# Kernel optimization log

Measured on AMD Instinct MI355X. Metric: run time of the kernel, lower is better.

## Reference

```python
import jax, jax.numpy as jnp
import numpy as np


def setup_inputs() -> dict:
    key = jax.random.key(0)
    k1, k2, k3 = jax.random.split(key, 3)
    B, d, N, T = 8, 256, 4096, 1024
    K = jax.random.normal(k1, (B, d, N), dtype=jnp.float32)
    V = jax.random.normal(k2, (B, d, N), dtype=jnp.float32)
    Q = jax.random.normal(k3, (B, d, T), dtype=jnp.float32)
    return {"K": K, "V": V, "Q": Q}


def reference(K, V, Q):
    d = K.shape[1]
    scale = 1.0 / jnp.sqrt(jnp.asarray(d, dtype=K.dtype))
    # scores: (B, N, T) = K^T @ Q
    scores = jnp.einsum('bdn,bdt->bnt', K, Q) * scale
    A = jax.nn.softmax(scores, axis=1)  # softmax over keys N
    R = jnp.einsum('bdn,bnt->bdt', V, A)  # (B, d, T)
    R_ = jnp.concatenate((R, Q), axis=1)  # (B, 2d, T)
    maxAtt = jnp.argmax(A, axis=1)  # (B, T)
    return (R_, A, maxAtt)
```

## Files before the change

### kernel.cpp

```cpp
#include <hip/hip_runtime.h>
#include <cfloat>

#define BB 8
#define DD 256
#define NN 4096
#define TT 1024
constexpr float SCALE = 0.0625f;

typedef __attribute__((ext_vector_type(8))) short bf16x8;
typedef __attribute__((ext_vector_type(4))) float f32x4;
typedef __attribute__((ext_vector_type(8))) unsigned short u16x8;

__device__ inline unsigned short f2bf(float x) {
  union { float f; unsigned u; } v; v.f = x;
  unsigned r = v.u + 0x7fff + ((v.u >> 16) & 1);
  return (unsigned short)(r >> 16);
}
__device__ inline float bf2f(unsigned short h) {
  union { unsigned u; float f; } v; v.u = ((unsigned)h) << 16;
  return v.f;
}

__device__ inline void glds16(const unsigned short* g, const short* lbase) {
  __builtin_amdgcn_global_load_lds((const __attribute__((address_space(1))) unsigned int*)g,
                                   (__attribute__((address_space(3))) unsigned int*)lbase,
                                   16, 0, 0);
}

__device__ inline void wg_barrier() {
  __builtin_amdgcn_sched_barrier(0);
  __builtin_amdgcn_s_barrier();
  __builtin_amdgcn_sched_barrier(0);
}

#define MPART_OFF 0u
#define LPART_OFF (1u << 20)
#define IPART_OFF (2u << 20)
#define MARR_OFF  (3u << 20)
#define RLARR_OFF ((3u << 20) + 32768u)
#define CONV_OFF  (4u << 20)
#define KT_HI_OFF (CONV_OFF)
#define KT_LO_OFF (CONV_OFF + 16777216u)
#define QT_HI_OFF (CONV_OFF + 33554432u)
#define QT_LO_OFF (CONV_OFF + 37748736u)
#define VH_OFF    (CONV_OFF + 41943040u)
#define RPART_OFF (CONV_OFF)
#define WS_NEED   (62914560ull)

__global__ __launch_bounds__(256) void convert_all(const float* __restrict__ Ksrc,
                                                   const float* __restrict__ Qsrc,
                                                   const float* __restrict__ Vsrc,
                                                   unsigned short* __restrict__ KHi,
                                                   unsigned short* __restrict__ KLo,
                                                   unsigned short* __restrict__ QHi,
                                                   unsigned short* __restrict__ QLo,
                                                   unsigned short* __restrict__ Vh) {
  __shared__ float tile[64][65];
  const int bx = blockIdx.x;
  const int b = blockIdx.z;
  const int tid = threadIdx.x;

  if (bx >= 80) {
    const int y = blockIdx.y;
    size_t g = (((size_t)b * 4 + y) * 256 + (bx - 80)) * 256 + tid;
    float4 v = ((const float4*)Vsrc)[g];
    unsigned short h[4] = {f2bf(v.x), f2bf(v.y), f2bf(v.z), f2bf(v.w)};
    *(ushort4*)(Vh + g * 4) = *(ushort4*)h;
    return;
  }

  const int d0 = blockIdx.y * 64;
  const float* src; unsigned short* dhi; unsigned short* dlo; int C; int c0;
  if (bx < 64) { src = Ksrc; dhi = KHi; dlo = KLo; C = NN; c0 = bx * 64; }
  else         { src = Qsrc; dhi = QHi; dlo = QLo; C = TT; c0 = (bx - 64) * 64; }
  const float* s = src + ((size_t)b * DD + d0) * C + c0;
  const int r = tid >> 4, cg = (tid & 15) * 4;
#pragma unroll
  for (int it = 0; it < 4; ++it) {
    float4 v = *(const float4*)(s + (size_t)(r + it * 16) * C + cg);
    tile[r + it * 16][cg + 0] = v.x; tile[r + it * 16][cg + 1] = v.y;
    tile[r + it * 16][cg + 2] = v.z; tile[r + it * 16][cg + 3] = v.w;
  }
  __syncthreads();
  const int cl = tid >> 2, dg = (tid & 3) * 16;
  unsigned short hi[16], lo[16];
#pragma unroll
  for (int j = 0; j < 16; ++j) {
    float x = tile[dg + j][cl];
    unsigned short h = f2bf(x);
    hi[j] = h;
    lo[j] = f2bf(x - bf2f(h));
  }
  size_t off = ((size_t)b * C + c0 + cl) * DD + d0 + dg;
  *(u16x8*)(dhi + off) = *(u16x8*)&hi[0];
  *(u16x8*)(dhi + off + 8) = *(u16x8*)&hi[8];
  *(u16x8*)(dlo + off) = *(u16x8*)&lo[0];
  *(u16x8*)(dlo + off + 8) = *(u16x8*)&lo[8];
}

__global__ __launch_bounds__(256) void gemm_scores_mfma(const unsigned short* __restrict__ KtHi,
                                                        const unsigned short* __restrict__ KtLo,
                                                        const unsigned short* __restrict__ QtHi,
                                                        const unsigned short* __restrict__ QtLo,
                                                        float* __restrict__ S,
                                                        float* __restrict__ mPart,
                                                        float* __restrict__ lPart,
                                                        int* __restrict__ iPart) {
  __shared__ __align__(16) short sAhi[2][128 * 32];
  __shared__ __align__(16) short sAlo[2][128 * 32];
  __shared__ __align__(16) short sBhi[2][128 * 32];
  __shared__ __align__(16) short sBlo[2][128 * 32];
  __shared__ float sm[256], sl[256];
  __shared__ int si[256];

  const int lin = blockIdx.x + ((blockIdx.y + (blockIdx.z << 5)) << 3);
  const int wg = ((lin & 7) << 8) + (lin >> 3);
  const int b = wg >> 8;
  const int cy = (wg >> 3) & 31;
  const int n0 = cy * 128;
  const int t0 = (wg & 7) * 128;
  const int tid = threadIdx.x;
  const int lane = tid & 63, w = tid >> 6;
  const int nh = (w & 1) * 64, th = (w >> 1) * 64;
  const int fr = lane & 15, q = lane >> 4;

  const unsigned short* aHi = KtHi + ((size_t)b * NN + n0) * DD;
  const unsigned short* aLo = KtLo + ((size_t)b * NN + n0) * DD;
  const unsigned short* bHi = QtHi + ((size_t)b * TT + t0) * DD;
  const unsigned short* bLo = QtLo + ((size_t)b * TT + t0) * DD;

  f32x4 acc[4][4];
#pragma unroll
  for (int i = 0; i < 4; ++i)
#pragma unroll
    for (int j = 0; j < 4; ++j) acc[i][j] = (f32x4){0.f, 0.f, 0.f, 0.f};

  const int Rr = lane >> 2;
  const int Qq = (lane & 3) ^ ((lane >> 3) & 3);
  const size_t s0 = (size_t)((w * 2 + 0) * 16 + Rr) * DD + Qq * 8;
  const size_t s1 = (size_t)((w * 2 + 1) * 16 + Rr) * DD + Qq * 8;
  const int g0 = (w * 2 + 0) * 512;
  const int g1 = (w * 2 + 1) * 512;
  const int pq8 = (q ^ ((fr >> 1) & 3)) * 8;

#define STAGE_K1(buf, kk)                         \
    glds16(aHi + s0 + (kk), &sAhi[buf][g0]);      \
    glds16(aHi + s1 + (kk), &sAhi[buf][g1]);      \
    glds16(aLo + s0 + (kk), &sAlo[buf][g0]);      \
    glds16(aLo + s1 + (kk), &sAlo[buf][g1]);      \
    glds16(bHi + s0 + (kk), &sBhi[buf][g0]);      \
    glds16(bHi + s1 + (kk), &sBhi[buf][g1]);      \
    glds16(bLo + s0 + (kk), &sBlo[buf][g0]);      \
    glds16(bLo + s1 + (kk), &sBlo[buf][g1]);

  STAGE_K1(0, 0);

  for (int step = 0; step < 8; ++step) {
    const int bi = step & 1;
    if (step < 7) {
      STAGE_K1(bi ^ 1, (step + 1) * 32);
      __builtin_amdgcn_sched_barrier(0);
      asm volatile("s_waitcnt vmcnt(8)" ::: "memory");
    } else {
      __builtin_amdgcn_sched_barrier(0);
      asm volatile("s_waitcnt vmcnt(0)" ::: "memory");
    }
    wg_barrier();

    bf16x8 bh[4], bl[4];
#pragma unroll
    for (int tb = 0; tb < 4; ++tb) {
      int off = (((w >> 1) * 4 + tb) * 512) + fr * 32 + pq8;
      bh[tb] = *(const bf16x8*)&sBhi[bi][off];
      bl[tb] = *(const bf16x8*)&sBlo[bi][off];
    }
#pragma unroll
    for (int mb = 0; mb < 4; ++mb) {
      int off = (((w & 1) * 4 + mb) * 512) + fr * 32 + pq8;
      bf16x8 ah = *(const bf16x8*)&sAhi[bi][off];
      bf16x8 al = *(const bf16x8*)&sAlo[bi][off];
#pragma unroll
      for (int tb = 0; tb < 4; ++tb) {
        acc[mb][tb] = __builtin_amdgcn_mfma_f32_16x16x32_bf16(ah, bh[tb], acc[mb][tb], 0, 0, 0);
        acc[mb][tb] = __builtin_amdgcn_mfma_f32_16x16x32_bf16(ah, bl[tb], acc[mb][tb], 0, 0, 0);
        acc[mb][tb] = __builtin_amdgcn_mfma_f32_16x16x32_bf16(al, bh[tb], acc[mb][tb], 0, 0, 0);
      }
    }
    wg_barrier();
  }
#undef STAGE_K1

#pragma unroll
  for (int tb = 0; tb < 4; ++tb) {
    const int tl = th + tb * 16 + fr;
    const int t = t0 + tl;
    float tmp[16];
    float m = -FLT_MAX; int id = 0;
#pragma unroll
    for (int mb = 0; mb < 4; ++mb)
#pragma unroll
      for (int r = 0; r < 4; ++r) {
        float v = acc[mb][tb][r] * SCALE;
        int n = n0 + nh + mb * 16 + q * 4 + r;
        S[((size_t)b * NN + n) * TT + t] = v;
        tmp[mb * 4 + r] = v;
        int nl = nh + mb * 16 + q * 4 + r;
        if (v > m) { m = v; id = nl; }
      }
    float l = 0.f;
#pragma unroll
    for (int j = 0; j < 16; ++j) l += __expf(tmp[j] - m);
#pragma unroll
    for (int off = 16; off <= 32; off <<= 1) {
      float m2 = __shfl_xor(m, off);
      float l2 = __shfl_xor(l, off);
      int i2 = __shfl_xor(id, off);
      if (m2 > m)       { l = l * __expf(m - m2) + l2; m = m2; id = i2; }
      else if (m2 == m) { l += l2; id = min(id, i2); }
      else              { l += l2 * __expf(m2 - m); }
    }
    if (q == 0) {
      int slot = (w & 1) * 128 + tl;
      sm[slot] = m; sl[slot] = l; si[slot] = id;
    }
  }
  __syncthreads();
  if (tid < 128) {
    float m = sm[tid], l = sl[tid]; int id = si[tid];
    float m2 = sm[128 + tid], l2 = sl[128 + tid]; int i2 = si[128 + tid];
    if (m2 > m)       { l = l * __expf(m - m2) + l2; m = m2; id = i2; }
    else if (m2 == m) { l += l2; id = min(id, i2); }
    else              { l += l2 * __expf(m2 - m); }
    size_t p = ((size_t)b * 32 + cy) * TT + t0 + tid;
    mPart[p] = m; lPart[p] = l; iPart[p] = n0 + id;
  }
}

__global__ __launch_bounds__(256) void gemm_out_fused2(const unsigned short* __restrict__ Vh,
                                                       float* __restrict__ A,
                                                       const float* __restrict__ mPart,
                                                       const float* __restrict__ lPart,
                                                       const int* __restrict__ iPart,
                                                       float* __restrict__ Rpart,
                                                       float* __restrict__ outMax) {
  __shared__ __align__(16) short sV[2][256 * 32];
  __shared__ __align__(16) short sA[32 * 40];
  __shared__ float rsm[8][32], rsl[8][32];
  __shared__ int   rsi[8][32];
  __shared__ float sm[32], srl[32];

  const int lin = blockIdx.x + (blockIdx.y << 5) + (blockIdx.z << 7);
  const int b  = lin & 7;
  const int ny = (lin >> 3) & 3;
  const int t0 = ((lin >> 5) & 31) * 32;

  const int tid = threadIdx.x;
  const int lane = tid & 63, w = tid >> 6;
  const int fr = lane & 15, q = lane >> 4, fk = q * 8;
  const int sn = tid >> 3, tg = tid & 7;

  const unsigned short* Vb = Vh + (size_t)b * DD * NN;
  float* Ab = A + (size_t)b * NN * TT;
  float* Arow = Ab + (size_t)sn * TT + t0 + tg * 4;

  const int Rr = lane >> 2;
  const int Qq = (lane & 3) ^ ((lane >> 3) & 3);
  const unsigned short* vsrc = Vb + (size_t)(w * 64 + Rr) * NN + Qq * 8;
  const int pq8 = (q ^ ((fr >> 1) & 3)) * 8;
  const int n0 = ny * 1024;

#pragma unroll
  for (int c = 0; c < 4; ++c)
    glds16(vsrc + (size_t)(c * 16) * NN + n0, &sV[0][(w * 4 + c) * 512]);
  float4 cur = *(const float4*)(Arow + (size_t)n0 * TT);

  {
    const int tl = tid & 31, g = tid >> 5;
    float m = -FLT_MAX, l = 0.f; int idx = 0;
#pragma unroll
    for (int cc = 0; cc < 4; ++cc) {
      size_t p = ((size_t)b * 32 + g * 4 + cc) * TT + t0 + tl;
      float m2 = mPart[p], l2 = lPart[p]; int i2 = iPart[p];
      if (m2 > m)       { l = l * __expf(m - m2) + l2; m = m2; idx = i2; }
      else if (m2 == m) { l += l2; idx = min(idx, i2); }
      else              { l += l2 * __expf(m2 - m); }
    }
    rsm[g][tl] = m; rsl[g][tl] = l; rsi[g][tl] = idx;
  }
  __syncthreads();
  if (tid < 32) {
    float m = rsm[0][tid], l = rsl[0][tid]; int idx = rsi[0][tid];
#pragma unroll
    for (int g = 1; g < 8; ++g) {
      float m2 = rsm[g][tid], l2 = rsl[g][tid]; int i2 = rsi[g][tid];
      if (m2 > m)       { l = l * __expf(m - m2) + l2; m = m2; idx = i2; }
      else if (m2 == m) { l += l2; idx = min(idx, i2); }
      else              { l += l2 * __expf(m2 - m); }
    }
    sm[tid] = m; srl[tid] = 1.0f / l;
    if (ny == 0) outMax[(size_t)b * TT + t0 + tid] = (float)idx;
  }
  asm volatile("s_waitcnt vmcnt(0)" ::: "memory");
  __syncthreads();

  const float4 mv = *(const float4*)&sm[tg * 4];
  const float4 rv = *(const float4*)&srl[tg * 4];

  f32x4 acc[4][2];
#pragma unroll
  for (int i = 0; i < 4; ++i) { acc[i][0] = (f32x4){0,0,0,0}; acc[i][1] = (f32x4){0,0,0,0}; }

  for (int it = 0; it < 31; ++it) {
    const int nn = n0 + it * 32;
    const int bi = it & 1;
#pragma unroll
    for (int c = 0; c < 4; ++c)
      glds16(vsrc + (size_t)(c * 16) * NN + (nn + 32), &sV[bi ^ 1][(w * 4 + c) * 512]);
    float4 nxt = *(const float4*)(Arow + (size_t)(nn + 32) * TT);

    float4 av;
    av.x = __expf(cur.x - mv.x) * rv.x;
    av.y = __expf(cur.y - mv.y) * rv.y;
    av.z = __expf(cur.z - mv.z) * rv.z;
    av.w = __expf(cur.w - mv.w) * rv.w;
    *(float4*)(Arow + (size_t)nn * TT) = av;
    sA[(tg * 4 + 0) * 40 + sn] = (short)f2bf(av.x);
    sA[(tg * 4 + 1) * 40 + sn] = (short)f2bf(av.y);
    sA[(tg * 4 + 2) * 40 + sn] = (short)f2bf(av.z);
    sA[(tg * 4 + 3) * 40 + sn] = (short)f2bf(av.w);

    __builtin_amdgcn_sched_barrier(0);
    asm volatile("s_waitcnt vmcnt(8) lgkmcnt(0)" ::: "memory");
    wg_barrier();

    bf16x8 bf0 = *(const bf16x8*)&sA[(0 * 16 + fr) * 40 + fk];
    bf16x8 bf1 = *(const bf16x8*)&sA[(1 * 16 + fr) * 40 + fk];
#pragma unroll
    for (int mb = 0; mb < 4; ++mb) {
      bf16x8 af = *(const bf16x8*)&sV[bi][w * 2048 + mb * 512 + fr * 32 + pq8];
      acc[mb][0] = __builtin_amdgcn_mfma_f32_16x16x32_bf16(af, bf0, acc[mb][0], 0, 0, 0);
      acc[mb][1] = __builtin_amdgcn_mfma_f32_16x16x32_bf16(af, bf1, acc[mb][1], 0, 0, 0);
    }
    wg_barrier();
    cur = nxt;
  }

  {
    const int nn = n0 + 992;
    float4 av;
    av.x = __expf(cur.x - mv.x) * rv.x;
    av.y = __expf(cur.y - mv.y) * rv.y;
    av.z = __expf(cur.z - mv.z) * rv.z;
    av.w = __expf(cur.w - mv.w) * rv.w;
    *(float4*)(Arow + (size_t)nn * TT) = av;
    sA[(tg * 4 + 0) * 40 + sn] = (short)f2bf(av.x);
    sA[(tg * 4 + 1) * 40 + sn] = (short)f2bf(av.y);
    sA[(tg * 4 + 2) * 40 + sn] = (short)f2bf(av.z);
    sA[(tg * 4 + 3) * 40 + sn] = (short)f2bf(av.w);

    __builtin_amdgcn_sched_barrier(0);
    asm volatile("s_waitcnt vmcnt(0) lgkmcnt(0)" ::: "memory");
    wg_barrier();

    bf16x8 bf0 = *(const bf16x8*)&sA[(0 * 16 + fr) * 40 + fk];
    bf16x8 bf1 = *(const bf16x8*)&sA[(1 * 16 + fr) * 40 + fk];
#pragma unroll
    for (int mb = 0; mb < 4; ++mb) {
      bf16x8 af = *(const bf16x8*)&sV[1][w * 2048 + mb * 512 + fr * 32 + pq8];
      acc[mb][0] = __builtin_amdgcn_mfma_f32_16x16x32_bf16(af, bf0, acc[mb][0], 0, 0, 0);
      acc[mb][1] = __builtin_amdgcn_mfma_f32_16x16x32_bf16(af, bf1, acc[mb][1], 0, 0, 0);
    }
  }

#pragma unroll
  for (int mb = 0; mb < 4; ++mb)
#pragma unroll
    for (int tb = 0; tb < 2; ++tb) {
      const int t = t0 + tb * 16 + fr;
#pragma unroll
      for (int r = 0; r < 4; ++r) {
        const int d = w * 64 + mb * 16 + q * 4 + r;
        Rpart[(((size_t)b * 4 + ny) * DD + d) * TT + t] = acc[mb][tb][r];
      }
    }
}

__global__ __launch_bounds__(256) void combine(const float* __restrict__ Rpart,
                                               const float* __restrict__ Qp,
                                               float* __restrict__ out) {
  const int lin = blockIdx.x;
  const int b = lin & 7;
  const int d = lin >> 3;
  const int t = threadIdx.x * 4;
  if (d < 256) {
    float4 s0 = *(const float4*)(Rpart + (((size_t)b * 4 + 0) * DD + d) * TT + t);
    float4 s1 = *(const float4*)(Rpart + (((size_t)b * 4 + 1) * DD + d) * TT + t);
    float4 s2 = *(const float4*)(Rpart + (((size_t)b * 4 + 2) * DD + d) * TT + t);
    float4 s3 = *(const float4*)(Rpart + (((size_t)b * 4 + 3) * DD + d) * TT + t);
    float4 r = make_float4(s0.x + s1.x + s2.x + s3.x, s0.y + s1.y + s2.y + s3.y,
                           s0.z + s1.z + s2.z + s3.z, s0.w + s1.w + s2.w + s3.w);
    *(float4*)(out + ((size_t)b * 512 + d) * TT + t) = r;
  } else {
    float4 v = *(const float4*)(Qp + ((size_t)b * 256 + (d - 256)) * TT + t);
    *(float4*)(out + ((size_t)b * 512 + d) * TT + t) = v;
  }
}

__global__ __launch_bounds__(256) void gemm_scores_fp32(const float* __restrict__ Kp,
                                                        const float* __restrict__ Qp,
                                                        float* __restrict__ S) {
  const int b = blockIdx.z;
  const int n0 = blockIdx.y * 128;
  const int t0 = blockIdx.x * 128;
  const int tid = threadIdx.x;
  const int tx = tid & 15, ty = tid >> 4;
  __shared__ float Kt[8][128];
  __shared__ float Qt[8][128];
  float acc[8][8];
#pragma unroll
  for (int i = 0; i < 8; ++i)
#pragma unroll
    for (int j = 0; j < 8; ++j) acc[i][j] = 0.f;
  const int lin = tid * 4;
  const int lkk = lin >> 7, lcol = lin & 127;
  const float* Kbase = Kp + (size_t)b * DD * NN;
  const float* Qbase = Qp + (size_t)b * DD * TT;
  for (int dd0 = 0; dd0 < DD; dd0 += 8) {
    float4 kv = *(const float4*)(Kbase + (size_t)(dd0 + lkk) * NN + n0 + lcol);
    float4 qv = *(const float4*)(Qbase + (size_t)(dd0 + lkk) * TT + t0 + lcol);
    __syncthreads();
    *(float4*)&Kt[lkk][lcol] = kv;
    *(float4*)&Qt[lkk][lcol] = qv;
    __syncthreads();
#pragma unroll
    for (int kk = 0; kk < 8; ++kk) {
      float4 a0 = *(float4*)&Kt[kk][ty * 4];
      float4 a1 = *(float4*)&Kt[kk][64 + ty * 4];
      float4 b0 = *(float4*)&Qt[kk][tx * 4];
      float4 b1 = *(float4*)&Qt[kk][64 + tx * 4];
      float av[8] = {a0.x, a0.y, a0.z, a0.w, a1.x, a1.y, a1.z, a1.w};
      float bv[8] = {b0.x, b0.y, b0.z, b0.w, b1.x, b1.y, b1.z, b1.w};
#pragma unroll
      for (int i = 0; i < 8; ++i)
#pragma unroll
        for (int j = 0; j < 8; ++j) acc[i][j] += av[i] * bv[j];
    }
  }
#pragma unroll
  for (int i = 0; i < 8; ++i) {
    int r = n0 + ((i < 4) ? (ty * 4 + i) : (64 + ty * 4 + i - 4));
    float* dst = S + ((size_t)b * NN + r) * TT + t0;
    *(float4*)(dst + tx * 4) = make_float4(acc[i][0] * SCALE, acc[i][1] * SCALE, acc[i][2] * SCALE, acc[i][3] * SCALE);
    *(float4*)(dst + 64 + tx * 4) = make_float4(acc[i][4] * SCALE, acc[i][5] * SCALE, acc[i][6] * SCALE, acc[i][7] * SCALE);
  }
}

__global__ __launch_bounds__(256) void stats_partial_fb(const float* __restrict__ S,
                                                        float* __restrict__ mPart,
                                                        float* __restrict__ lPart,
                                                        int* __restrict__ iPart) {
  const int tid = threadIdx.x;
  const int tx = tid & 63, ty = tid >> 6;
  const int b = blockIdx.z;
  const int t = blockIdx.x * 64 + tx;
  const int nbase = blockIdx.y * 512;
  float m = -FLT_MAX, l = 0.f;
  int idx = 0;
  const float* col = S + (size_t)b * NN * TT + t;
  for (int n = nbase + ty; n < nbase + 512; n += 4) {
    float s = col[(size_t)n * TT];
    if (s > m) { l = l * __expf(m - s) + 1.0f; m = s; idx = n; }
    else        l += __expf(s - m);
  }
  __shared__ float sm[4][64], sl[4][64];
  __shared__ int si[4][64];
  sm[ty][tx] = m; sl[ty][tx] = l; si[ty][tx] = idx;
  __syncthreads();
  if (ty == 0) {
#pragma unroll
    for (int k = 1; k < 4; ++k) {
      float m2 = sm[k][tx], l2 = sl[k][tx];
      int i2 = si[k][tx];
      if (m2 > m)       { l = l * __expf(m - m2) + l2; m = m2; idx = i2; }
      else if (m2 == m) { l += l2; idx = min(idx, i2); }
      else              { l += l2 * __expf(m2 - m); }
    }
    size_t p = (size_t)(b * 8 + blockIdx.y) * TT + t;
    mPart[p] = m; lPart[p] = l; iPart[p] = idx;
  }
}

__global__ __launch_bounds__(256) void stats_final_fb(const float* __restrict__ mPart,
                                                      const float* __restrict__ lPart,
                                                      const int* __restrict__ iPart,
                                                      float* __restrict__ mArr,
                                                      float* __restrict__ rlArr,
                                                      float* __restrict__ outMax) {
  int col = blockIdx.x * 256 + threadIdx.x;
  int b = col >> 10, t = col & 1023;
  float m = -FLT_MAX, l = 0.f;
  int idx = 0;
#pragma unroll
  for (int c = 0; c < 8; ++c) {
    size_t p = (size_t)(b * 8 + c) * TT + t;
    float m2 = mPart[p], l2 = lPart[p];
    int i2 = iPart[p];
    if (m2 > m)       { l = l * __expf(m - m2) + l2; m = m2; idx = i2; }
    else if (m2 == m) { l += l2; idx = min(idx, i2); }
    else              { l += l2 * __expf(m2 - m); }
  }
  mArr[col] = m;
  rlArr[col] = 1.0f / l;
  outMax[col] = (float)idx;
}

__global__ __launch_bounds__(256) void normalize_fb(float* __restrict__ A,
                                                    const float* __restrict__ mArr,
                                                    const float* __restrict__ rlArr) {
  int g = blockIdx.x * 256 + threadIdx.x;
  float4 s = ((const float4*)A)[g];
  int e = g * 4;
  int t0 = e & 1023;
  int row = e >> 10;
  int b = row >> 12;
  int cb = (b << 10) + t0;
  float4 r;
  r.x = __expf(s.x - mArr[cb + 0]) * rlArr[cb + 0];
  r.y = __expf(s.y - mArr[cb + 1]) * rlArr[cb + 1];
  r.z = __expf(s.z - mArr[cb + 2]) * rlArr[cb + 2];
  r.w = __expf(s.w - mArr[cb + 3]) * rlArr[cb + 3];
  ((float4*)A)[g] = r;
}

__global__ __launch_bounds__(256) void gemm_out_fp32(const float* __restrict__ Vp,
                                                     const float* __restrict__ A,
                                                     float* __restrict__ Rout) {
  const int b = blockIdx.z;
  const int m0 = blockIdx.y * 64;
  const int t0 = blockIdx.x * 128;
  const int tid = threadIdx.x;
  const int tx = tid & 15, ty = tid >> 4;
  __shared__ float Vt[16][68];
  __shared__ float At[16][128];
  float acc[4][8];
#pragma unroll
  for (int i = 0; i < 4; ++i)
#pragma unroll
    for (int j = 0; j < 8; ++j) acc[i][j] = 0.f;
  const float* Vbase = Vp + (size_t)b * DD * NN;
  const float* Abase = A + (size_t)b * NN * TT;
  const int vmm = tid >> 2, vkk = (tid & 3) * 4;
  const int akk = tid >> 5, att = (tid * 4) & 127;
  for (int nn0 = 0; nn0 < NN; nn0 += 16) {
    float4 vv = *(const float4*)(Vbase + (size_t)(m0 + vmm) * NN + nn0 + vkk);
    float4 a0 = *(const float4*)(Abase + (size_t)(nn0 + akk) * TT + t0 + att);
    float4 a1 = *(const float4*)(Abase + (size_t)(nn0 + akk + 8) * TT + t0 + att);
    __syncthreads();
    Vt[vkk + 0][vmm] = vv.x; Vt[vkk + 1][vmm] = vv.y;
    Vt[vkk + 2][vmm] = vv.z; Vt[vkk + 3][vmm] = vv.w;
    *(float4*)&At[akk][att] = a0;
    *(float4*)&At[akk + 8][att] = a1;
    __syncthreads();
#pragma unroll
    for (int kk = 0; kk < 16; ++kk) {
      float4 a4 = *(float4*)&Vt[kk][ty * 4];
      float4 b0 = *(float4*)&At[kk][tx * 4];
      float4 b1 = *(float4*)&At[kk][64 + tx * 4];
      float av[4] = {a4.x, a4.y, a4.z, a4.w};
      float bv[8] = {b0.x, b0.y, b0.z, b0.w, b1.x, b1.y, b1.z, b1.w};
#pragma unroll
      for (int i = 0; i < 4; ++i)
#pragma unroll
        for (int j = 0; j < 8; ++j) acc[i][j] += av[i] * bv[j];
    }
  }
#pragma unroll
  for (int i = 0; i < 4; ++i) {
    int r = m0 + ty * 4 + i;
    float* dst = Rout + (size_t)b * (2 * DD) * TT + (size_t)r * TT + t0;
    *(float4*)(dst + tx * 4) = make_float4(acc[i][0], acc[i][1], acc[i][2], acc[i][3]);
    *(float4*)(dst + 64 + tx * 4) = make_float4(acc[i][4], acc[i][5], acc[i][6], acc[i][7]);
  }
}

__global__ __launch_bounds__(256) void qcopy(const float* __restrict__ Qp,
                                             float* __restrict__ out) {
  int g = blockIdx.x * 256 + threadIdx.x;
  int e = g * 4;
  int t0 = e & 1023;
  int row = e >> 10;
  int dd = row & 255, b = row >> 8;
  float4 v = ((const float4*)Qp)[g];
  *(float4*)(out + (size_t)b * 512 * TT + (size_t)(256 + dd) * TT + t0) = v;
}

extern "C" void kernel_launch(void* const* d_in, const int* in_sizes, int n_in,
                              void* d_out, int out_size, void* d_ws, size_t ws_size,
                              hipStream_t stream) {
  const float* Kp = (const float*)d_in[0];
  const float* Vp = (const float*)d_in[1];
  const float* Qp = (const float*)d_in[2];
  float* out = (float*)d_out;
  float* R_ = out;
  float* A = out + 4194304;
  float* outMax = out + 4194304 + 33554432;

  char* wsb = (char*)d_ws;
  float* mPart = (float*)(wsb + MPART_OFF);
  float* lPart = (float*)(wsb + LPART_OFF);
  int*   iPart = (int*)(wsb + IPART_OFF);
  float* mArr  = (float*)(wsb + MARR_OFF);
  float* rlArr = (float*)(wsb + RLARR_OFF);

  const bool fast = (ws_size >= WS_NEED);

  if (fast) {
    unsigned short* KtHi = (unsigned short*)(wsb + KT_HI_OFF);
    unsigned short* KtLo = (unsigned short*)(wsb + KT_LO_OFF);
    unsigned short* QtHi = (unsigned short*)(wsb + QT_HI_OFF);
    unsigned short* QtLo = (unsigned short*)(wsb + QT_LO_OFF);
    unsigned short* Vh   = (unsigned short*)(wsb + VH_OFF);
    float* Rpart = (float*)(wsb + RPART_OFF);

    convert_all<<<dim3(336, 4, BB), 256, 0, stream>>>(Kp, Qp, Vp, KtHi, KtLo, QtHi, QtLo, Vh);
    gemm_scores_mfma<<<dim3(TT / 128, NN / 128, BB), 256, 0, stream>>>(
        KtHi, KtLo, QtHi, QtLo, A, mPart, lPart, iPart);
    gemm_out_fused2<<<dim3(TT / 32, 4, BB), 256, 0, stream>>>(
        Vh, A, mPart, lPart, iPart, Rpart, outMax);
    combine<<<dim3(4096), 256, 0, stream>>>(Rpart, Qp, R_);
  } else {
    gemm_scores_fp32<<<dim3(TT / 128, NN / 128, BB), 256, 0, stream>>>(Kp, Qp, A);
    stats_partial_fb<<<dim3(TT / 64, NN / 512, BB), 256, 0, stream>>>(A, mPart, lPart, iPart);
    stats_final_fb<<<dim3(32), 256, 0, stream>>>(mPart, lPart, iPart, mArr, rlArr, outMax);
    normalize_fb<<<dim3((BB * NN * TT / 4) / 256), 256, 0, stream>>>(A, mArr, rlArr);
    gemm_out_fp32<<<dim3(TT / 128, DD / 64, BB), 256, 0, stream>>>(Vp, A, R_);
    qcopy<<<dim3((BB * DD * TT / 4) / 256), 256, 0, stream>>>(Qp, R_);
  }
}
```

Before: 328.4 us.

## Stage score and partial-output stores through LDS for coalesced float4 writes

Both GEMM epilogues now write their MFMA accumulators into a padded LDS tile and then emit coalesced float4 rows to global memory. Before, each lane made scattered scalar stores with a large stride. To free LDS for this staging buffer, the scores GEMM drops its double-buffered global-to-LDS prefetch and uses a single buffer with plain __syncthreads. That removes the overlap between loads and MFMA work in the K loop and adds extra barriers in both epilogues.

Measured after the change: 339.0 us. 3.2% more time.

```diff
diff --git a/kernel.cpp b/kernel.cpp
--- a/kernel.cpp
+++ b/kernel.cpp
@@ -106,10 +106,12 @@
                                                         float* __restrict__ mPart,
                                                         float* __restrict__ lPart,
                                                         int* __restrict__ iPart) {
-  __shared__ __align__(16) short sAhi[2][128 * 32];
-  __shared__ __align__(16) short sAlo[2][128 * 32];
-  __shared__ __align__(16) short sBhi[2][128 * 32];
-  __shared__ __align__(16) short sBlo[2][128 * 32];
+  __shared__ __align__(16) char smem1[32768];
+  short* sAhi = (short*)&smem1[0];
+  short* sAlo = (short*)&smem1[8192];
+  short* sBhi = (short*)&smem1[16384];
+  short* sBlo = (short*)&smem1[24576];
+  float* strn = (float*)&smem1[0];
   __shared__ float sm[256], sl[256];
   __shared__ int si[256];
 
@@ -143,42 +145,29 @@
   const int g1 = (w * 2 + 1) * 512;
   const int pq8 = (q ^ ((fr >> 1) & 3)) * 8;
 
-#define STAGE_K1(buf, kk)                         \
-    glds16(aHi + s0 + (kk), &sAhi[buf][g0]);      \
-    glds16(aHi + s1 + (kk), &sAhi[buf][g1]);      \
-    glds16(aLo + s0 + (kk), &sAlo[buf][g0]);      \
-    glds16(aLo + s1 + (kk), &sAlo[buf][g1]);      \
-    glds16(bHi + s0 + (kk), &sBhi[buf][g0]);      \
-    glds16(bHi + s1 + (kk), &sBhi[buf][g1]);      \
-    glds16(bLo + s0 + (kk), &sBlo[buf][g0]);      \
-    glds16(bLo + s1 + (kk), &sBlo[buf][g1]);
-
-  STAGE_K1(0, 0);
-
-  for (int step = 0; step < 8; ++step) {
-    const int bi = step & 1;
-    if (step < 7) {
-      STAGE_K1(bi ^ 1, (step + 1) * 32);
-      __builtin_amdgcn_sched_barrier(0);
-      asm volatile("s_waitcnt vmcnt(8)" ::: "memory");
-    } else {
-      __builtin_amdgcn_sched_barrier(0);
-      asm volatile("s_waitcnt vmcnt(0)" ::: "memory");
-    }
-    wg_barrier();
+  for (int kk = 0; kk < DD; kk += 32) {
+    glds16(aHi + s0 + kk, sAhi + g0);
+    glds16(aHi + s1 + kk, sAhi + g1);
+    glds16(aLo + s0 + kk, sAlo + g0);
+    glds16(aLo + s1 + kk, sAlo + g1);
+    glds16(bHi + s0 + kk, sBhi + g0);
+    glds16(bHi + s1 + kk, sBhi + g1);
+    glds16(bLo + s0 + kk, sBlo + g0);
+    glds16(bLo + s1 + kk, sBlo + g1);
+    __syncthreads();
 
     bf16x8 bh[4], bl[4];
 #pragma unroll
     for (int tb = 0; tb < 4; ++tb) {
       int off = (((w >> 1) * 4 + tb) * 512) + fr * 32 + pq8;
-      bh[tb] = *(const bf16x8*)&sBhi[bi][off];
-      bl[tb] = *(const bf16x8*)&sBlo[bi][off];
+      bh[tb] = *(const bf16x8*)&sBhi[off];
+      bl[tb] = *(const bf16x8*)&sBlo[off];
     }
 #pragma unroll
     for (int mb = 0; mb < 4; ++mb) {
       int off = (((w & 1) * 4 + mb) * 512) + fr * 32 + pq8;
-      bf16x8 ah = *(const bf16x8*)&sAhi[bi][off];
-      bf16x8 al = *(const bf16x8*)&sAlo[bi][off];
+      bf16x8 ah = *(const bf16x8*)&sAhi[off];
+      bf16x8 al = *(const bf16x8*)&sAlo[off];
 #pragma unroll
       for (int tb = 0; tb < 4; ++tb) {
         acc[mb][tb] = __builtin_amdgcn_mfma_f32_16x16x32_bf16(ah, bh[tb], acc[mb][tb], 0, 0, 0);
@@ -186,14 +175,12 @@
         acc[mb][tb] = __builtin_amdgcn_mfma_f32_16x16x32_bf16(al, bh[tb], acc[mb][tb], 0, 0, 0);
       }
     }
-    wg_barrier();
-  }
-#undef STAGE_K1
+    __syncthreads();
+  }
 
 #pragma unroll
   for (int tb = 0; tb < 4; ++tb) {
     const int tl = th + tb * 16 + fr;
-    const int t = t0 + tl;
     float tmp[16];
     float m = -FLT_MAX; int id = 0;
 #pragma unroll
@@ -201,8 +188,6 @@
 #pragma unroll
       for (int r = 0; r < 4; ++r) {
         float v = acc[mb][tb][r] * SCALE;
-        int n = n0 + nh + mb * 16 + q * 4 + r;
-        S[((size_t)b * NN + n) * TT + t] = v;
         tmp[mb * 4 + r] = v;
         int nl = nh + mb * 16 + q * 4 + r;
         if (v > m) { m = v; id = nl; }
@@ -233,6 +218,29 @@
     else              { l += l2 * __expf(m2 - m); }
     size_t p = ((size_t)b * 32 + cy) * TT + t0 + tid;
     mPart[p] = m; lPart[p] = l; iPart[p] = n0 + id;
+  }
+
+  const int tlw = (w >> 1) * 16 + fr;
+#pragma unroll
+  for (int tb = 0; tb < 4; ++tb) {
+    __syncthreads();
+#pragma unroll
+    for (int mb = 0; mb < 4; ++mb)
+#pragma unroll
+      for (int r = 0; r < 4; ++r) {
+        int n = nh + mb * 16 + q * 4 + r;
+        strn[n * 36 + tlw] = acc[mb][tb][r] * SCALE;
+      }
+    __syncthreads();
+#pragma unroll
+    for (int i = 0; i < 4; ++i) {
+      int s = i * 256 + tid;
+      int row = s >> 3, c4 = s & 7;
+      float4 v = *(float4*)&strn[row * 36 + c4 * 4];
+      int tl0 = c4 * 4;
+      int t = t0 + ((tl0 < 16) ? (tb * 16 + tl0) : (64 + tb * 16 + (tl0 - 16)));
+      *(float4*)(S + ((size_t)b * NN + n0 + row) * TT + t) = v;
+    }
   }
 }
 
@@ -249,6 +257,8 @@
   __shared__ int   rsi[8][32];
   __shared__ float sm[32], srl[32];
 
+  float* strn = (float*)&sV[0][0];
+
   const int lin = blockIdx.x + (blockIdx.y << 5) + (blockIdx.z << 7);
   const int b  = lin & 7;
   const int ny = (lin >> 3) & 3;
@@ -372,17 +382,31 @@
     }
   }
 
-#pragma unroll
-  for (int mb = 0; mb < 4; ++mb)
-#pragma unroll
-    for (int tb = 0; tb < 2; ++tb) {
-      const int t = t0 + tb * 16 + fr;
-#pragma unroll
-      for (int r = 0; r < 4; ++r) {
-        const int d = w * 64 + mb * 16 + q * 4 + r;
-        Rpart[(((size_t)b * 4 + ny) * DD + d) * TT + t] = acc[mb][tb][r];
-      }
-    }
+  __syncthreads();
+#pragma unroll
+  for (int p = 0; p < 2; ++p) {
+    if ((w >> 1) == p) {
+      const int dbase = (w & 1) * 64;
+#pragma unroll
+      for (int mb = 0; mb < 4; ++mb)
+#pragma unroll
+        for (int tb = 0; tb < 2; ++tb)
+#pragma unroll
+          for (int r = 0; r < 4; ++r) {
+            int dloc = dbase + mb * 16 + q * 4 + r;
+            strn[dloc * 36 + tb * 16 + fr] = acc[mb][tb][r];
+          }
+    }
+    __syncthreads();
+#pragma unroll
+    for (int i = 0; i < 4; ++i) {
+      int s = i * 256 + tid;
+      int row = s >> 3, c4 = s & 7;
+      float4 v = *(float4*)&strn[row * 36 + c4 * 4];
+      *(float4*)(Rpart + (((size_t)b * 4 + ny) * DD + p * 128 + row) * TT + t0 + c4 * 4) = v;
+    }
+    __syncthreads();
+  }
 }
 
 __global__ __launch_bounds__(256) void combine(const float* __restrict__ Rpart,
```
